# Performance work log

Measured on AMD Instinct MI355X. Metric: run time of the kernel, lower is better.

## Reference

```python
import jax, jax.numpy as jnp
import numpy as np

N = 50000; E = 800000; G = 64
HID = 128; HEADS = 4; HC = HID // HEADS
L = 3; RESID_FREQ = 2
EPS = 1e-5; SLOPE = 0.2


def setup_inputs() -> dict:
    key = jax.random.key(0)
    ks = jax.random.split(key, 16)
    s = 1.0 / np.sqrt(HID)
    f = jnp.float32
    return {
        "x": jax.random.normal(ks[0], (N, HID), f),
        "edge_index": jax.random.randint(ks[1], (2, E), 0, N, dtype=jnp.int32),
        "batch": jnp.sort(jax.random.randint(ks[2], (N,), 0, G, dtype=jnp.int32)),
        "w_in1": jax.random.normal(ks[3], (HID, HID), f) * s,
        "b_in1": jnp.zeros((HID,), f),
        "w_in2": jax.random.normal(ks[4], (HID, HID), f) * s,
        "b_in2": jnp.zeros((HID,), f),
        "gat_w": jax.random.normal(ks[5], (L, HID, HID), f) * s,
        "gat_att_src": jax.random.normal(ks[6], (L, HEADS, HC), f) * s,
        "gat_att_dst": jax.random.normal(ks[7], (L, HEADS, HC), f) * s,
        "gat_b": jnp.zeros((L, HID), f),
        "gcn_w": jax.random.normal(ks[8], (L, HID, HID), f) * s,
        "gcn_b": jnp.zeros((L, HID), f),
        "norm_w": jnp.ones((L, HID), f),
        "norm_b": jnp.zeros((L, HID), f),
        "norm_ms": jnp.ones((L, HID), f),
        "skip_w": jax.random.normal(ks[9], (L, HID, HID), f) * s,
        "skip_b": jnp.zeros((L, HID), f),
        "w_h1": jax.random.normal(ks[10], (HID, HID), f) * s,
        "b_h1": jnp.zeros((HID,), f),
        "w_h2": jax.random.normal(ks[11], (HID, HID // 2), f) * s,
        "b_h2": jnp.zeros((HID // 2,), f),
        "w_h3": jax.random.normal(ks[12], (HID // 2, 1), f) * s,
        "b_h3": jnp.zeros((1,), f),
        "edge_w_param": jnp.ones((1,), f),
    }


def _gat(x, src, dst, w, a_src, a_dst, b):
    # PyG GATConv (eval): lin -> per-edge additive attention -> edge softmax over dst -> scatter-sum
    h = (x @ w).reshape(N, HEADS, HC)
    sc_src = jnp.sum(h * a_src, axis=-1)  # [N, H]
    sc_dst = jnp.sum(h * a_dst, axis=-1)
    alpha = jax.nn.leaky_relu(sc_src[src] + sc_dst[dst], SLOPE)  # [Ef, H]
    amax = jax.ops.segment_max(alpha, dst, num_segments=N)  # every node has a self-loop
    ex = jnp.exp(alpha - amax[dst])
    denom = jax.ops.segment_sum(ex, dst, num_segments=N)
    coef = ex / (denom[dst] + 1e-16)
    out = jax.ops.segment_sum(h[src] * coef[:, :, None], dst, num_segments=N)
    return out.reshape(N, HID) + b


def _gcn(x, src, dst, ew, w, b):
    # PyG GCNConv with improved=True (self-loop weight 2.0 already in ew): sym-normalized SpMM
    deg = jax.ops.segment_sum(ew, dst, num_segments=N)
    dinv = jnp.where(deg > 0, jax.lax.rsqrt(deg), 0.0)
    norm = dinv[src] * ew * dinv[dst]
    h = x @ w
    return jax.ops.segment_sum(h[src] * norm[:, None], dst, num_segments=N) + b


def _graph_norm(x, batch, w, b, ms):
    cnt = jax.ops.segment_sum(jnp.ones((N, 1), x.dtype), batch, num_segments=G)
    cnt = jnp.maximum(cnt, 1.0)
    mean = jax.ops.segment_sum(x, batch, num_segments=G) / cnt
    out = x - mean[batch] * ms
    var = jax.ops.segment_sum(out * out, batch, num_segments=G) / cnt
    return out / jnp.sqrt(var[batch] + EPS) * w + b


def reference(x, edge_index, batch, w_in1, b_in1, w_in2, b_in2, gat_w, gat_att_src,
              gat_att_dst, gat_b, gcn_w, gcn_b, norm_w, norm_b, norm_ms, skip_w,
              skip_b, w_h1, b_h1, w_h2, b_h2, w_h3, b_h3, edge_w_param):
    # undirected: concat reversed edges; then self-loops (added by both GAT and GCN convs)
    loop = jnp.arange(N, dtype=edge_index.dtype)
    src = jnp.concatenate([edge_index[0], edge_index[1], loop])
    dst = jnp.concatenate([edge_index[1], edge_index[0], loop])
    ew = jnp.concatenate([
        edge_w_param[0] * jnp.ones((2 * E,), x.dtype),
        2.0 * jnp.ones((N,), x.dtype),  # improved=True self-loop fill value
    ])
    h = jax.nn.relu(x @ w_in1 + b_in1) @ w_in2 + b_in2
    for i in range(L):
        prev = h
        g1 = _gat(h, src, dst, gat_w[i], gat_att_src[i], gat_att_dst[i], gat_b[i])
        g2 = _gcn(h, src, dst, ew, gcn_w[i], gcn_b[i])
        h = jax.nn.elu(_graph_norm(g1 + g2, batch, norm_w[i], norm_b[i], norm_ms[i]))
        if i % RESID_FREQ == 0:
            h = h + prev @ skip_w[i] + skip_b[i]
    p = jax.nn.relu(h @ w_h1 + b_h1)
    p = jax.nn.relu(p @ w_h2 + b_h2)
    return jax.nn.sigmoid(p @ w_h3 + b_h3).reshape(-1)
```

## Files before the change

kernel.cpp:

```cpp
#include <hip/hip_runtime.h>
#include <hip/hip_fp16.h>

typedef unsigned int uint;
typedef unsigned short ushort;
typedef __attribute__((ext_vector_type(8))) short short8;
typedef __attribute__((ext_vector_type(4))) float f32x4;
typedef __attribute__((ext_vector_type(2))) float f32x2;

#define N_NODES 50000
#define N_EDGES 800000
#define ETOT    (2 * N_EDGES + N_NODES)
#define NG      64
#define NBKT    256
#define MAXB    10240
#define EPB     8192
#define NBK1    ((ETOT + EPB - 1) / EPB)
#define AROW    640

__device__ __forceinline__ short f2bf(float f) {
  uint u = __float_as_uint(f);
  u += 0x7fffu + ((u >> 16) & 1u);
  return (short)(u >> 16);
}
__device__ __forceinline__ float bf2f(short s) {
  return __uint_as_float(((uint)(ushort)s) << 16);
}
__device__ __forceinline__ uint packbf(float a, float b) {
  return (uint)(ushort)f2bf(a) | ((uint)(ushort)f2bf(b) << 16);
}
__device__ __forceinline__ uint pkh2(float a, float b) {
  __half2 h = __floats2half2_rn(a, b);
  return *(uint*)&h;
}
__device__ __forceinline__ float2 uph2(uint u) {
  __half2 h = *(__half2*)&u;
  return __half22float2(h);
}

__global__ __launch_bounds__(256) void bucket_k(const int* __restrict__ ei,
                                                int* __restrict__ gfill,
                                                uint* __restrict__ est) {
  __shared__ int hist[NBKT];
  __shared__ int cursor[NBKT];
  const int tid = threadIdx.x;
  hist[tid] = 0;
  __syncthreads();
  const int e0 = blockIdx.x * EPB;
#pragma unroll 4
  for (int i = 0; i < EPB / 256; ++i) {
    int e = e0 + i * 256 + tid;
    if (e < ETOT) {
      int d;
      if (e < N_EDGES)          d = ei[N_EDGES + e];
      else if (e < 2 * N_EDGES) d = ei[e - N_EDGES];
      else                      d = e - 2 * N_EDGES;
      atomicAdd(&hist[d >> 8], 1);
    }
  }
  __syncthreads();
  cursor[tid] = atomicAdd(&gfill[tid], hist[tid]);
  __syncthreads();
#pragma unroll 4
  for (int i = 0; i < EPB / 256; ++i) {
    int e = e0 + i * 256 + tid;
    if (e < ETOT) {
      int s, d, fl = 0;
      if (e < N_EDGES)          { s = ei[e];           d = ei[N_EDGES + e]; }
      else if (e < 2 * N_EDGES) { s = ei[e];           d = ei[e - N_EDGES]; }
      else                      { s = e - 2 * N_EDGES; d = s; fl = 1; }
      int b = d >> 8;
      int slot = atomicAdd(&cursor[b], 1);
      est[(size_t)b * MAXB + slot] = (uint)s | ((uint)(d & 255) << 16) | ((uint)fl << 24);
    }
  }
}

__global__ __launch_bounds__(256) void group_k(const int* __restrict__ gfill,
                                               const uint* __restrict__ est,
                                               const float* __restrict__ ewp,
                                               int* __restrict__ csrc,
                                               int* __restrict__ rbeg,
                                               int* __restrict__ rend,
                                               float* __restrict__ dinv) {
  __shared__ int hist[NBKT];
  __shared__ int cursor[NBKT];
  __shared__ int wsum[4];
  __shared__ int bsum[4];
  const int b = blockIdx.x;
  const int tid = threadIdx.x;
  const int lane = tid & 63, wid = tid >> 6;
  const int cnt = gfill[b];
  {
    int vv = (tid < b) ? gfill[tid] : 0;
#pragma unroll
    for (int off = 32; off; off >>= 1) vv += __shfl_xor(vv, off, 64);
    if (lane == 0) bsum[wid] = vv;
  }
  hist[tid] = 0;
  __syncthreads();
  const int gb = bsum[0] + bsum[1] + bsum[2] + bsum[3];
  const uint* basep = est + (size_t)b * MAXB;
  for (int i = tid; i < cnt; i += 256)
    atomicAdd(&hist[(basep[i] >> 16) & 255], 1);
  __syncthreads();
  int v = hist[tid];
  int x = v;
#pragma unroll
  for (int d = 1; d < 64; d <<= 1) {
    int t = __shfl_up(x, d, 64);
    if (lane >= d) x += t;
  }
  if (lane == 63) wsum[wid] = x;
  __syncthreads();
  int woff = 0;
#pragma unroll
  for (int j = 0; j < 4; ++j) if (j < wid) woff += wsum[j];
  int excl = woff + x - v;
  cursor[tid] = excl;
  int node = b * 256 + tid;
  if (node < N_NODES) {
    rbeg[node] = gb + excl;
    rend[node] = gb + excl + v;
    float deg = ewp[0] * (float)(v - 1) + 2.0f;
    dinv[node] = (deg > 0.f) ? rsqrtf(deg) : 0.f;
  }
  __syncthreads();
  for (int i = tid; i < cnt; i += 256) {
    uint en = basep[i];
    int dlow = (en >> 16) & 255;
    int slot = atomicAdd(&cursor[dlow], 1);
    csrc[gb + slot] = (int)(en & 0xffffu) | (int)((en >> 24) << 31);
  }
}

__global__ __launch_bounds__(128) void gcnt_k(const int* __restrict__ batch,
                                              int* __restrict__ gcnt) {
  __shared__ int lb[NG + 1];
  int g = threadIdx.x;
  if (g <= NG) {
    int lo = 0, hi = N_NODES;
    while (lo < hi) {
      int mid = (lo + hi) >> 1;
      if (batch[mid] < g) lo = mid + 1; else hi = mid;
    }
    lb[g] = lo;
  }
  __syncthreads();
  if (g < NG) gcnt[g] = lb[g + 1] - lb[g];
}

__global__ __launch_bounds__(256) void prep_k(const float* __restrict__ w_in1,
                                              const float* __restrict__ w_in2,
                                              const float* __restrict__ gat_w,
                                              const float* __restrict__ gcn_w,
                                              const float* __restrict__ skip_w,
                                              const float* __restrict__ w_h1,
                                              const float* __restrict__ w_h2,
                                              short* __restrict__ WT0,
                                              short* __restrict__ WT1,
                                              short* __restrict__ WTL2,
                                              short* __restrict__ WTS,
                                              short* __restrict__ WTH1,
                                              short* __restrict__ WTH2) {
  int mat = blockIdx.x >> 2, qr = blockIdx.x & 3;
  const float* src; short* dst; int ncol = 128, dstride = 128, doff = 0;
  switch (mat) {
    case 0:  src = w_in1; dst = WT0; break;
    case 1:  src = w_in2; dst = WT1; break;
    case 2: case 3: case 4:
      src = gat_w + (size_t)(mat - 2) * 16384; dst = WTL2 + (size_t)(mat - 2) * 32768;
      dstride = 256; break;
    case 5: case 6: case 7:
      src = gcn_w + (size_t)(mat - 5) * 16384; dst = WTL2 + (size_t)(mat - 5) * 32768;
      dstride = 256; doff = 128; break;
    case 8:  src = skip_w;             dst = WTS;         break;
    case 9:  src = skip_w + 2 * 16384; dst = WTS + 16384; break;
    case 10: src = w_h1; dst = WTH1; break;
    default: src = w_h2; dst = WTH2; ncol = 64; break;
  }
  int total = 128 * ncol, chunk = total / 4;
  for (int d = qr * chunk + threadIdx.x; d < (qr + 1) * chunk; d += 256) {
    int col = d >> 7, k = d & 127;
    dst[col * dstride + doff + k] = f2bf(src[k * ncol + col]);
  }
}

__global__ __launch_bounds__(256) void attprep_k(const float* __restrict__ gat_w,
                                                 const float* __restrict__ asrc,
                                                 const float* __restrict__ adst,
                                                 const float* __restrict__ gat_b,
                                                 const float* __restrict__ gcn_b,
                                                 short* __restrict__ ATTW,
                                                 float* __restrict__ BSUM) {
  const int tid = threadIdx.x;
  for (int t = tid; t < 3072; t += 256) {
    int l = t >> 10, rem = t & 1023;
    int r = rem >> 7, k = rem & 127;
    int hd = r & 3;
    const float* av = (r < 4) ? (asrc + l * 128 + hd * 32) : (adst + l * 128 + hd * 32);
    const float* wrow = gat_w + (size_t)l * 16384 + k * 128 + hd * 32;
    float s = 0.f;
#pragma unroll
    for (int c = 0; c < 32; ++c) s = fmaf(wrow[c], av[c], s);
    ATTW[(size_t)l * 2048 + r * 128 + k] = f2bf(s);
  }
  for (int t = tid; t < 3072; t += 256)
    ATTW[(size_t)(t >> 10) * 2048 + 1024 + (t & 1023)] = 0;
  for (int t = tid; t < 384; t += 256) {
    int l = t >> 7, c = t & 127;
    BSUM[t] = gat_b[l * 128 + c] + gcn_b[l * 128 + c];
  }
}

template <int NCOL, int RELU, int F32OUT, int AF32, int NORM>
__global__ __launch_bounds__(256) void bgemm_k(const short* __restrict__ A,
                                               const float* __restrict__ Af,
                                               const short* __restrict__ WT,
                                               const float* __restrict__ bias,
                                               const short* __restrict__ gb_,
                                               const int* __restrict__ batch,
                                               const int* __restrict__ gcnt,
                                               const float* __restrict__ gsum,
                                               const float* __restrict__ nw,
                                               const float* __restrict__ nb_,
                                               const float* __restrict__ nms,
                                               short* __restrict__ outb,
                                               float* __restrict__ outf, int M) {
  constexpr int NT = NCOL / 16;
  const int lane = threadIdx.x & 63;
  const int wid = threadIdx.x >> 6;
  const int mbase = blockIdx.x * 64 + wid * 16;
  const int l15 = lane & 15, q = lane >> 4;
  int arow = mbase + l15; if (arow > M - 1) arow = M - 1;
  const short* bp = WT + (size_t)l15 * 128 + q * 8;
  f32x4 acc[NT];
#pragma unroll
  for (int t = 0; t < NT; ++t) acc[t] = (f32x4)0.f;
#pragma unroll
  for (int c = 0; c < 4; ++c) {
    short8 av;
    if (AF32) {
      const float* apf = Af + (size_t)arow * 128 + q * 8 + c * 32;
      float4 fa = *(const float4*)apf;
      float4 fb = *(const float4*)(apf + 4);
      uint2 lo = make_uint2(packbf(fa.x, fa.y), packbf(fa.z, fa.w));
      uint2 hi = make_uint2(packbf(fb.x, fb.y), packbf(fb.z, fb.w));
      uint4 all = make_uint4(lo.x, lo.y, hi.x, hi.y);
      av = *(short8*)&all;
    } else {
      av = *(const short8*)(A + (size_t)arow * 128 + q * 8 + c * 32);
    }
#pragma unroll
    for (int t = 0; t < NT; ++t) {
      short8 bv = *(const short8*)(bp + (size_t)t * 16 * 128 + c * 32);
      acc[t] = __builtin_amdgcn_mfma_f32_16x16x32_bf16(av, bv, acc[t], 0, 0, 0);
    }
  }
#pragma unroll
  for (int t = 0; t < NT; ++t) {
    int col = t * 16 + l15;
    float bb = bias ? bias[col] : 0.f;
#pragma unroll
    for (int r = 0; r < 4; ++r) {
      int row = mbase + q * 4 + r;
      if (row < M) {
        float v = acc[t][r] + bb;
        if (NORM) {
          int b = batch[row];
          float cinv = 1.0f / fmaxf((float)gcnt[b], 1.0f);
          float mean = gsum[b * 256 + col] * cinv;
          float msq  = gsum[b * 256 + 128 + col] * cinv;
          float ms = nms[col];
          float var = fmaxf(msq - (2.0f * ms - ms * ms) * mean * mean, 0.f);
          float g = bf2f(gb_[(size_t)row * AROW + col]);
          float tn = (g - mean * ms) * rsqrtf(var + 1e-5f) * nw[col] + nb_[col];
          tn = (tn > 0.f) ? tn : (__expf(tn) - 1.0f);
          v += tn;
        }
        if (RELU) v = v > 0.f ? v : 0.f;
        if (F32OUT) outf[(size_t)row * NCOL + col] = v;
        else        outb[(size_t)row * NCOL + col] = f2bf(v);
      }
    }
  }
}

__global__ __launch_bounds__(256) void agg_k(const short* __restrict__ h,
                                             const float* __restrict__ sc,
                                             const int* __restrict__ rbeg,
                                             const int* __restrict__ rend,
                                             const int* __restrict__ cs,
                                             const float* __restrict__ dinv,
                                             const float* __restrict__ ewp,
                                             short* __restrict__ A) {
  __shared__ uint4 lco[4][64];
  const int n = blockIdx.x * 4 + (threadIdx.x >> 6);
  const int wv = threadIdx.x >> 6;
  const int l = threadIdx.x & 63;
  const int sub = l >> 5;
  const int f4 = l & 31;
  const float ew0 = ewp[0];
  const float dn = dinv[n];
  const f32x4 sdv = *(const f32x4*)(sc + n * 16 + 4);
  const int beg = rbeg[n], end = rend[n];
  float den[4] = {0.f, 0.f, 0.f, 0.f};
  f32x2 ag[4][2], ac[2];
#pragma unroll
  for (int hd = 0; hd < 4; ++hd) { ag[hd][0] = (f32x2)0.f; ag[hd][1] = (f32x2)0.f; }
  ac[0] = (f32x2)0.f; ac[1] = (f32x2)0.f;

  for (int c0 = beg; c0 < end; c0 += 64) {
    const int nc = min(64, end - c0);
    {
      uint4 w = make_uint4(0u, 0u, 0u, 0u);
      int e = c0 + l;
      if (e < end) {
        int raw = cs[e];
        int s = raw & 0x7fffffff;
        float wt = (raw < 0) ? 2.0f : ew0;
        f32x4 ssv = *(const f32x4*)(sc + (size_t)s * 16);
        float a0 = ssv[0] + sdv[0]; a0 = fmaxf(a0, 0.2f * a0);
        float a1 = ssv[1] + sdv[1]; a1 = fmaxf(a1, 0.2f * a1);
        float a2 = ssv[2] + sdv[2]; a2 = fmaxf(a2, 0.2f * a2);
        float a3 = ssv[3] + sdv[3]; a3 = fmaxf(a3, 0.2f * a3);
        float e0 = __expf(a0), e1 = __expf(a1);
        float e2 = __expf(a2), e3 = __expf(a3);
        den[0] += e0; den[1] += e1; den[2] += e2; den[3] += e3;
        float c2 = dinv[s] * wt * dn;
        __half hc = __float2half(c2);
        w = make_uint4(pkh2(e0, e1), pkh2(e2, e3),
                       (uint)(*(ushort*)&hc) | ((uint)s << 16), 0u);
      }
      lco[wv][l] = w;
    }
    const int pairs = (nc + 1) & ~1;
#pragma unroll 2
    for (int j = sub; j < pairs; j += 2) {
      uint4 cw = lco[wv][j];
      int s = (int)(cw.z >> 16);
      float2 p01 = uph2(cw.x);
      float2 p23 = uph2(cw.y);
      ushort hc = (ushort)(cw.z & 0xffffu);
      float c2 = __half2float(*(__half*)&hc);
      uint2 u = *(const uint2*)(h + (size_t)s * 128 + f4 * 4);
      f32x2 va, vb;
      va.x = __uint_as_float(u.x << 16);
      va.y = __uint_as_float(u.x & 0xffff0000u);
      vb.x = __uint_as_float(u.y << 16);
      vb.y = __uint_as_float(u.y & 0xffff0000u);
      f32x2 cc;
      cc.x = p01.x; cc.y = p01.x;
      ag[0][0] += cc * va; ag[0][1] += cc * vb;
      cc.x = p01.y; cc.y = p01.y;
      ag[1][0] += cc * va; ag[1][1] += cc * vb;
      cc.x = p23.x; cc.y = p23.x;
      ag[2][0] += cc * va; ag[2][1] += cc * vb;
      cc.x = p23.y; cc.y = p23.y;
      ag[3][0] += cc * va; ag[3][1] += cc * vb;
      cc.x = c2; cc.y = c2;
      ac[0] += cc * va; ac[1] += cc * vb;
    }
  }

#pragma unroll
  for (int off = 1; off < 64; off <<= 1) {
    den[0] += __shfl_xor(den[0], off, 64);
    den[1] += __shfl_xor(den[1], off, 64);
    den[2] += __shfl_xor(den[2], off, 64);
    den[3] += __shfl_xor(den[3], off, 64);
  }
#pragma unroll
  for (int hd = 0; hd < 4; ++hd)
#pragma unroll
    for (int i = 0; i < 2; ++i) {
      f32x2 t = ag[hd][i];
      t.x += __shfl_xor(t.x, 32, 64);
      t.y += __shfl_xor(t.y, 32, 64);
      ag[hd][i] = t;
    }
#pragma unroll
  for (int i = 0; i < 2; ++i) {
    f32x2 t = ac[i];
    t.x += __shfl_xor(t.x, 32, 64);
    t.y += __shfl_xor(t.y, 32, 64);
    ac[i] = t;
  }

  float inv[4] = {1.0f / (den[0] + 1e-16f), 1.0f / (den[1] + 1e-16f),
                  1.0f / (den[2] + 1e-16f), 1.0f / (den[3] + 1e-16f)};
  short* base = A + (size_t)n * AROW;
  if (sub == 0) {
#pragma unroll
    for (int hd = 0; hd < 2; ++hd) {
      float iv = inv[hd];
      *(uint2*)(base + hd * 128 + f4 * 4) =
          make_uint2(packbf(ag[hd][0].x * iv, ag[hd][0].y * iv),
                     packbf(ag[hd][1].x * iv, ag[hd][1].y * iv));
    }
    *(uint2*)(base + 512 + f4 * 4) =
        make_uint2(packbf(ac[0].x, ac[0].y), packbf(ac[1].x, ac[1].y));
  } else {
#pragma unroll
    for (int hd = 2; hd < 4; ++hd) {
      float iv = inv[hd];
      *(uint2*)(base + hd * 128 + f4 * 4) =
          make_uint2(packbf(ag[hd][0].x * iv, ag[hd][0].y * iv),
                     packbf(ag[hd][1].x * iv, ag[hd][1].y * iv));
    }
  }
}

__global__ __launch_bounds__(256) void aggproj_k(const short* A,
                                                 const short* __restrict__ WT,
                                                 const float* __restrict__ bsum,
                                                 short* GB, int M) {
  const int lane = threadIdx.x & 63;
  const int wid = threadIdx.x >> 6;
  const int mbase = blockIdx.x * 64 + wid * 16;
  const int l15 = lane & 15, q = lane >> 4;
  int arow = mbase + l15; if (arow > M - 1) arow = M - 1;
  const short* ap = A + (size_t)arow * AROW + q * 8;
  const short* bp = WT + (size_t)l15 * 256 + q * 8;
  f32x4 acc[8];
#pragma unroll
  for (int t = 0; t < 8; ++t) acc[t] = (f32x4)0.f;
  short8 avg[4];
#pragma unroll
  for (int c = 0; c < 4; ++c) avg[c] = *(const short8*)(ap + 512 + c * 32);
#pragma unroll
  for (int hd = 0; hd < 4; ++hd) {
    short8 avh[4];
#pragma unroll
    for (int c = 0; c < 4; ++c) avh[c] = *(const short8*)(ap + hd * 128 + c * 32);
#pragma unroll
    for (int tt = 0; tt < 2; ++tt) {
      int t = hd * 2 + tt;
      const short* bpt = bp + (size_t)t * 16 * 256;
#pragma unroll
      for (int c = 0; c < 4; ++c) {
        short8 bv = *(const short8*)(bpt + c * 32);
        acc[t] = __builtin_amdgcn_mfma_f32_16x16x32_bf16(avh[c], bv, acc[t], 0, 0, 0);
      }
#pragma unroll
      for (int c = 0; c < 4; ++c) {
        short8 bv = *(const short8*)(bpt + 128 + c * 32);
        acc[t] = __builtin_amdgcn_mfma_f32_16x16x32_bf16(avg[c], bv, acc[t], 0, 0, 0);
      }
    }
  }
#pragma unroll
  for (int t = 0; t < 8; ++t) {
    int col = t * 16 + l15;
    float bb = bsum[col];
#pragma unroll
    for (int r = 0; r < 4; ++r) {
      int row = mbase + q * 4 + r;
      if (row < M) GB[(size_t)row * AROW + col] = f2bf(acc[t][r] + bb);
    }
  }
}

__global__ __launch_bounds__(256) void stats_k(const short* __restrict__ gb,
                                               const int* __restrict__ batch,
                                               float* __restrict__ gsum) {
  int c2 = threadIdx.x & 63;
  int qr = threadIdx.x >> 6;
  int nb = blockIdx.x * 16;
  float s0 = 0.f, s1 = 0.f, q0 = 0.f, q1 = 0.f;
  int curb = -1;
  for (int i = qr; i < 16; i += 4) {
    int n = nb + i;
    int b = batch[n];
    if (b != curb) {
      if (curb >= 0) {
        atomicAdd(&gsum[curb * 256 + 2 * c2], s0);
        atomicAdd(&gsum[curb * 256 + 2 * c2 + 1], s1);
        atomicAdd(&gsum[curb * 256 + 128 + 2 * c2], q0);
        atomicAdd(&gsum[curb * 256 + 128 + 2 * c2 + 1], q1);
      }
      curb = b; s0 = s1 = q0 = q1 = 0.f;
    }
    uint u = *(const uint*)(gb + (size_t)n * AROW + 2 * c2);
    float v0 = __uint_as_float(u << 16);
    float v1 = __uint_as_float(u & 0xffff0000u);
    s0 += v0; q0 = fmaf(v0, v0, q0);
    s1 += v1; q1 = fmaf(v1, v1, q1);
  }
  if (curb >= 0) {
    atomicAdd(&gsum[curb * 256 + 2 * c2], s0);
    atomicAdd(&gsum[curb * 256 + 2 * c2 + 1], s1);
    atomicAdd(&gsum[curb * 256 + 128 + 2 * c2], q0);
    atomicAdd(&gsum[curb * 256 + 128 + 2 * c2 + 1], q1);
  }
}

__global__ __launch_bounds__(256) void normelu_k(const short* __restrict__ gb,
                                                 const int* __restrict__ batch,
                                                 const float* __restrict__ gsum,
                                                 const int* __restrict__ gcnt,
                                                 const float* __restrict__ nw,
                                                 const float* __restrict__ nb_,
                                                 const float* __restrict__ nms,
                                                 short* __restrict__ outb) {
  int n = blockIdx.x * 4 + (threadIdx.x >> 6);
  int c2 = threadIdx.x & 63;
  int b = batch[n];
  float cntf = fmaxf((float)gcnt[b], 1.0f);
  float cinv = 1.0f / cntf;
  uint u = *(const uint*)(gb + (size_t)n * AROW + 2 * c2);
  float o[2];
#pragma unroll
  for (int k = 0; k < 2; ++k) {
    int c = 2 * c2 + k;
    float mean = gsum[b * 256 + c] * cinv;
    float msq  = gsum[b * 256 + 128 + c] * cinv;
    float ms = nms[c];
    float var = fmaxf(msq - (2.0f * ms - ms * ms) * mean * mean, 0.f);
    float v = (k == 0) ? __uint_as_float(u << 16) : __uint_as_float(u & 0xffff0000u);
    float t = (v - mean * ms) * rsqrtf(var + 1e-5f) * nw[c] + nb_[c];
    o[k] = (t > 0.f) ? t : (__expf(t) - 1.0f);
  }
  *(uint*)(outb + (size_t)n * 128 + 2 * c2) = packbf(o[0], o[1]);
}

__global__ __launch_bounds__(256) void head3_k(const short* __restrict__ p2,
                                               const float* __restrict__ w3,
                                               const float* __restrict__ b3,
                                               float* __restrict__ out) {
  int n = blockIdx.x * 4 + (threadIdx.x >> 6);
  int k = threadIdx.x & 63;
  float v = bf2f(p2[(size_t)n * 64 + k]) * w3[k];
#pragma unroll
  for (int off = 32; off; off >>= 1) v += __shfl_down(v, off, 64);
  if (k == 0) out[n] = 1.0f / (1.0f + __expf(-(v + b3[0])));
}

extern "C" void kernel_launch(void* const* d_in, const int* in_sizes, int n_in,
                              void* d_out, int out_size, void* d_ws, size_t ws_size,
                              hipStream_t stream) {
  const float* x      = (const float*)d_in[0];
  const int*   ei     = (const int*)d_in[1];
  const int*   batch  = (const int*)d_in[2];
  const float* w_in1  = (const float*)d_in[3];
  const float* b_in1  = (const float*)d_in[4];
  const float* w_in2  = (const float*)d_in[5];
  const float* b_in2  = (const float*)d_in[6];
  const float* gat_w  = (const float*)d_in[7];
  const float* gat_as = (const float*)d_in[8];
  const float* gat_ad = (const float*)d_in[9];
  const float* gat_b  = (const float*)d_in[10];
  const float* gcn_w  = (const float*)d_in[11];
  const float* gcn_b  = (const float*)d_in[12];
  const float* norm_w = (const float*)d_in[13];
  const float* norm_b = (const float*)d_in[14];
  const float* norm_ms= (const float*)d_in[15];
  const float* skip_w = (const float*)d_in[16];
  const float* skip_b = (const float*)d_in[17];
  const float* w_h1   = (const float*)d_in[18];
  const float* b_h1   = (const float*)d_in[19];
  const float* w_h2   = (const float*)d_in[20];
  const float* b_h2   = (const float*)d_in[21];
  const float* w_h3   = (const float*)d_in[22];
  const float* b_h3   = (const float*)d_in[23];
  const float* ewp    = (const float*)d_in[24];
  float* out = (float*)d_out;

  char* p = (char*)d_ws;
  const size_t NBH = (size_t)N_NODES * 128 * sizeof(short);
  short* B0   = (short*)p; p += NBH;
  short* B1   = (short*)p; p += NBH;
  short* MEGA = (short*)p; p += (size_t)N_NODES * AROW * sizeof(short);
  short* GB   = MEGA;
  uint*  EST  = (uint*)MEGA;
  float* SC   = (float*)p; p += (size_t)N_NODES * 16 * sizeof(float);
  int*   CSRC = (int*)p;   p += (size_t)ETOT * sizeof(int);
  int*   RBEG = (int*)p;   p += (size_t)N_NODES * sizeof(int);
  int*   REND = (int*)p;   p += (size_t)N_NODES * sizeof(int);
  char*  zbase = p;
  int*   GFILL= (int*)p;   p += (size_t)NBKT * sizeof(int);
  float* GSUM = (float*)p; p += (size_t)3 * NG * 256 * sizeof(float);
  size_t znb  = (size_t)((char*)p - zbase);
  int*   GCNT = (int*)p;   p += (size_t)NG * sizeof(int);
  float* DINV = (float*)p; p += (size_t)N_NODES * sizeof(float);
  short* WT0  = (short*)p; p += 16384 * sizeof(short);
  short* WT1  = (short*)p; p += 16384 * sizeof(short);
  short* WTL2 = (short*)p; p += 3 * 32768 * sizeof(short);
  short* WTS  = (short*)p; p += 2 * 16384 * sizeof(short);
  short* WTH1 = (short*)p; p += 16384 * sizeof(short);
  short* WTH2 = (short*)p; p += 8192 * sizeof(short);
  short* ATTW = (short*)p; p += 3 * 2048 * sizeof(short);
  float* BSUM = (float*)p; p += 3 * 128 * sizeof(float);

  const int GB_ = (N_NODES + 63) / 64;
  const short* nullb = nullptr;

  hipMemsetAsync(zbase, 0, znb, stream);
  bucket_k<<<NBK1, 256, 0, stream>>>(ei, GFILL, EST);
  group_k<<<196, 256, 0, stream>>>(GFILL, EST, ewp, CSRC, RBEG, REND, DINV);
  gcnt_k<<<1, 128, 0, stream>>>(batch, GCNT);
  prep_k<<<48, 256, 0, stream>>>(w_in1, w_in2, gat_w, gcn_w, skip_w, w_h1, w_h2,
                                 WT0, WT1, WTL2, WTS, WTH1, WTH2);
  attprep_k<<<1, 256, 0, stream>>>(gat_w, gat_as, gat_ad, gat_b, gcn_b, ATTW, BSUM);

  bgemm_k<128, 1, 0, 1, 0><<<GB_, 256, 0, stream>>>(nullb, x, WT0, b_in1,
      nullb, nullptr, nullptr, nullptr, nullptr, nullptr, nullptr, B1, nullptr, N_NODES);
  bgemm_k<128, 0, 0, 0, 0><<<GB_, 256, 0, stream>>>(B1, nullptr, WT1, b_in2,
      nullb, nullptr, nullptr, nullptr, nullptr, nullptr, nullptr, B0, nullptr, N_NODES);

  short* h = B0;
  for (int i = 0; i < 3; ++i) {
    short* hn = (h == B0) ? B1 : B0;
    float* gsum_i = GSUM + (size_t)i * NG * 256;
    const float* nw  = norm_w  + (size_t)i * 128;
    const float* nb  = norm_b  + (size_t)i * 128;
    const float* nms = norm_ms + (size_t)i * 128;
    bgemm_k<16, 0, 1, 0, 0><<<GB_, 256, 0, stream>>>(h, nullptr,
        ATTW + (size_t)i * 2048, nullptr, nullb, nullptr, nullptr, nullptr,
        nullptr, nullptr, nullptr, nullptr, SC, N_NODES);
    agg_k<<<N_NODES / 4, 256, 0, stream>>>(h, SC, RBEG, REND, CSRC, DINV, ewp, MEGA);
    aggproj_k<<<GB_, 256, 0, stream>>>(MEGA, WTL2 + (size_t)i * 32768,
                                       BSUM + i * 128, GB, N_NODES);
    stats_k<<<N_NODES / 16, 256, 0, stream>>>(GB, batch, gsum_i);
    if (i == 1) {
      normelu_k<<<N_NODES / 4, 256, 0, stream>>>(GB, batch, gsum_i, GCNT,
                                                 nw, nb, nms, hn);
    } else {
      const short* wts = WTS + (size_t)(i == 0 ? 0 : 1) * 16384;
      bgemm_k<128, 0, 0, 0, 1><<<GB_, 256, 0, stream>>>(h, nullptr, wts,
          skip_b + (size_t)i * 128, GB, batch, GCNT, gsum_i, nw, nb, nms,
          hn, nullptr, N_NODES);
    }
    h = hn;
  }

  bgemm_k<128, 1, 0, 0, 0><<<GB_, 256, 0, stream>>>(h, nullptr, WTH1, b_h1,
      nullb, nullptr, nullptr, nullptr, nullptr, nullptr, nullptr, B0, nullptr, N_NODES);
  bgemm_k<64, 1, 0, 0, 0><<<GB_, 256, 0, stream>>>(B0, nullptr, WTH2, b_h2,
      nullb, nullptr, nullptr, nullptr, nullptr, nullptr, nullptr, MEGA, nullptr, N_NODES);
  head3_k<<<N_NODES / 4, 256, 0, stream>>>(MEGA, w_h3, b_h3, out);
}
```

Baseline: 856.0 us.

## Fuse input MLP and head GEMMs, merge prep kernels, stage edge bucketing in LDS

The two input-MLP GEMMs become one kernel that keeps the hidden layer in shared memory, and the head's three stages (two GEMMs plus the final dot product and sigmoid) become one kernel. The three small prep kernels are merged into a single launch. Edge bucketing now handles only the real edges: self-loops are written directly by group_k, and entries are staged in LDS in bucket order so the global writes are contiguous. The goal is fewer launches, no intermediate activation round-trips through global memory, and more coalesced scatter writes, at the cost of extra shared-memory use and more complex index bookkeeping.

Result: faster. 813.3 us (-5.0%).

```diff
diff --git a/kernel.cpp b/kernel.cpp
--- a/kernel.cpp
+++ b/kernel.cpp
@@ -9,12 +9,13 @@
 
 #define N_NODES 50000
 #define N_EDGES 800000
+#define EREAL   (2 * N_EDGES)
 #define ETOT    (2 * N_EDGES + N_NODES)
 #define NG      64
 #define NBKT    256
 #define MAXB    10240
 #define EPB     8192
-#define NBK1    ((ETOT + EPB - 1) / EPB)
+#define NBK1    ((EREAL + EPB - 1) / EPB)
 #define AROW    640
 
 __device__ __forceinline__ short f2bf(float f) {
@@ -41,37 +42,54 @@
                                                 int* __restrict__ gfill,
                                                 uint* __restrict__ est) {
   __shared__ int hist[NBKT];
-  __shared__ int cursor[NBKT];
+  __shared__ int scan_[NBKT];
+  __shared__ int cur[NBKT];
+  __shared__ int claim[NBKT];
+  __shared__ int wsum[4];
+  __shared__ uint stage[EPB];
   const int tid = threadIdx.x;
   hist[tid] = 0;
   __syncthreads();
   const int e0 = blockIdx.x * EPB;
-#pragma unroll 4
-  for (int i = 0; i < EPB / 256; ++i) {
-    int e = e0 + i * 256 + tid;
-    if (e < ETOT) {
-      int d;
-      if (e < N_EDGES)          d = ei[N_EDGES + e];
-      else if (e < 2 * N_EDGES) d = ei[e - N_EDGES];
-      else                      d = e - 2 * N_EDGES;
-      atomicAdd(&hist[d >> 8], 1);
-    }
-  }
-  __syncthreads();
-  cursor[tid] = atomicAdd(&gfill[tid], hist[tid]);
-  __syncthreads();
-#pragma unroll 4
-  for (int i = 0; i < EPB / 256; ++i) {
-    int e = e0 + i * 256 + tid;
-    if (e < ETOT) {
-      int s, d, fl = 0;
-      if (e < N_EDGES)          { s = ei[e];           d = ei[N_EDGES + e]; }
-      else if (e < 2 * N_EDGES) { s = ei[e];           d = ei[e - N_EDGES]; }
-      else                      { s = e - 2 * N_EDGES; d = s; fl = 1; }
-      int b = d >> 8;
-      int slot = atomicAdd(&cursor[b], 1);
-      est[(size_t)b * MAXB + slot] = (uint)s | ((uint)(d & 255) << 16) | ((uint)fl << 24);
-    }
+  const int ecnt = min(EPB, EREAL - e0);
+  for (int i = tid; i < ecnt; i += 256) {
+    int e = e0 + i;
+    int d = (e < N_EDGES) ? ei[N_EDGES + e] : ei[e - N_EDGES];
+    atomicAdd(&hist[d >> 8], 1);
+  }
+  __syncthreads();
+  {
+    int v = hist[tid];
+    int lane = tid & 63, wid = tid >> 6;
+    int x = v;
+#pragma unroll
+    for (int d = 1; d < 64; d <<= 1) {
+      int t = __shfl_up(x, d, 64);
+      if (lane >= d) x += t;
+    }
+    if (lane == 63) wsum[wid] = x;
+    __syncthreads();
+    int woff = 0;
+#pragma unroll
+    for (int j = 0; j < 4; ++j) if (j < wid) woff += wsum[j];
+    scan_[tid] = woff + x - v;
+    cur[tid] = woff + x - v;
+    claim[tid] = atomicAdd(&gfill[tid], v);
+  }
+  __syncthreads();
+  for (int i = tid; i < ecnt; i += 256) {
+    int e = e0 + i;
+    int s = ei[e];
+    int d = (e < N_EDGES) ? ei[N_EDGES + e] : ei[e - N_EDGES];
+    int p = atomicAdd(&cur[d >> 8], 1);
+    stage[p] = (uint)s | ((uint)d << 16);
+  }
+  __syncthreads();
+  for (int p = tid; p < ecnt; p += 256) {
+    uint en = stage[p];
+    int b = en >> 24;
+    int gpos = claim[b] + (p - scan_[b]);
+    est[(size_t)b * MAXB + gpos] = en;
   }
 }
 
@@ -98,7 +116,7 @@
   }
   hist[tid] = 0;
   __syncthreads();
-  const int gb = bsum[0] + bsum[1] + bsum[2] + bsum[3];
+  const int gb = bsum[0] + bsum[1] + bsum[2] + bsum[3] + b * 256;
   const uint* basep = est + (size_t)b * MAXB;
   for (int i = tid; i < cnt; i += 256)
     atomicAdd(&hist[(basep[i] >> 16) & 255], 1);
@@ -116,12 +134,14 @@
 #pragma unroll
   for (int j = 0; j < 4; ++j) if (j < wid) woff += wsum[j];
   int excl = woff + x - v;
-  cursor[tid] = excl;
+  cursor[tid] = excl + tid + 1;
   int node = b * 256 + tid;
   if (node < N_NODES) {
-    rbeg[node] = gb + excl;
-    rend[node] = gb + excl + v;
-    float deg = ewp[0] * (float)(v - 1) + 2.0f;
+    int rs = gb + excl + tid;
+    rbeg[node] = rs;
+    rend[node] = rs + v + 1;
+    csrc[rs] = node | (int)0x80000000;
+    float deg = ewp[0] * (float)v + 2.0f;
     dinv[node] = (deg > 0.f) ? rsqrtf(deg) : 0.f;
   }
   __syncthreads();
@@ -129,39 +149,67 @@
     uint en = basep[i];
     int dlow = (en >> 16) & 255;
     int slot = atomicAdd(&cursor[dlow], 1);
-    csrc[gb + slot] = (int)(en & 0xffffu) | (int)((en >> 24) << 31);
-  }
-}
-
-__global__ __launch_bounds__(128) void gcnt_k(const int* __restrict__ batch,
-                                              int* __restrict__ gcnt) {
+    csrc[gb + slot] = (int)(en & 0xffffu);
+  }
+}
+
+__global__ __launch_bounds__(256) void prepall_k(const float* __restrict__ w_in1,
+                                                 const float* __restrict__ w_in2,
+                                                 const float* __restrict__ gat_w,
+                                                 const float* __restrict__ gcn_w,
+                                                 const float* __restrict__ skip_w,
+                                                 const float* __restrict__ w_h1,
+                                                 const float* __restrict__ w_h2,
+                                                 const float* __restrict__ asrc,
+                                                 const float* __restrict__ adst,
+                                                 const float* __restrict__ gat_b,
+                                                 const float* __restrict__ gcn_b,
+                                                 const int* __restrict__ batch,
+                                                 short* __restrict__ WT0,
+                                                 short* __restrict__ WT1,
+                                                 short* __restrict__ WTL2,
+                                                 short* __restrict__ WTS,
+                                                 short* __restrict__ WTH1,
+                                                 short* __restrict__ WTH2,
+                                                 short* __restrict__ ATTW,
+                                                 float* __restrict__ BSUM,
+                                                 int* __restrict__ gcnt) {
   __shared__ int lb[NG + 1];
-  int g = threadIdx.x;
-  if (g <= NG) {
-    int lo = 0, hi = N_NODES;
-    while (lo < hi) {
-      int mid = (lo + hi) >> 1;
-      if (batch[mid] < g) lo = mid + 1; else hi = mid;
-    }
-    lb[g] = lo;
-  }
-  __syncthreads();
-  if (g < NG) gcnt[g] = lb[g + 1] - lb[g];
-}
-
-__global__ __launch_bounds__(256) void prep_k(const float* __restrict__ w_in1,
-                                              const float* __restrict__ w_in2,
-                                              const float* __restrict__ gat_w,
-                                              const float* __restrict__ gcn_w,
-                                              const float* __restrict__ skip_w,
-                                              const float* __restrict__ w_h1,
-                                              const float* __restrict__ w_h2,
-                                              short* __restrict__ WT0,
-                                              short* __restrict__ WT1,
-                                              short* __restrict__ WTL2,
-                                              short* __restrict__ WTS,
-                                              short* __restrict__ WTH1,
-                                              short* __restrict__ WTH2) {
+  const int tid = threadIdx.x;
+  if (blockIdx.x == 48) {
+    for (int t = tid; t < 3072; t += 256) {
+      int l = t >> 10, rem = t & 1023;
+      int r = rem >> 7, k = rem & 127;
+      int hd = r & 3;
+      const float* av = (r < 4) ? (asrc + l * 128 + hd * 32) : (adst + l * 128 + hd * 32);
+      const float* wrow = gat_w + (size_t)l * 16384 + k * 128 + hd * 32;
+      float s = 0.f;
+#pragma unroll
+      for (int c = 0; c < 32; ++c) s = fmaf(wrow[c], av[c], s);
+      ATTW[(size_t)l * 2048 + r * 128 + k] = f2bf(s);
+    }
+    for (int t = tid; t < 3072; t += 256)
+      ATTW[(size_t)(t >> 10) * 2048 + 1024 + (t & 1023)] = 0;
+    for (int t = tid; t < 384; t += 256) {
+      int l = t >> 7, c = t & 127;
+      BSUM[t] = gat_b[l * 128 + c] + gcn_b[l * 128 + c];
+    }
+    return;
+  }
+  if (blockIdx.x == 49) {
+    int g = tid;
+    if (g <= NG) {
+      int lo = 0, hi = N_NODES;
+      while (lo < hi) {
+        int mid = (lo + hi) >> 1;
+        if (batch[mid] < g) lo = mid + 1; else hi = mid;
+      }
+      lb[g] = lo;
+    }
+    __syncthreads();
+    if (g < NG) gcnt[g] = lb[g + 1] - lb[g];
+    return;
+  }
   int mat = blockIdx.x >> 2, qr = blockIdx.x & 3;
   const float* src; short* dst; int ncol = 128, dstride = 128, doff = 0;
   switch (mat) {
@@ -179,42 +227,14 @@
     default: src = w_h2; dst = WTH2; ncol = 64; break;
   }
   int total = 128 * ncol, chunk = total / 4;
-  for (int d = qr * chunk + threadIdx.x; d < (qr + 1) * chunk; d += 256) {
+  for (int d = qr * chunk + tid; d < (qr + 1) * chunk; d += 256) {
     int col = d >> 7, k = d & 127;
     dst[col * dstride + doff + k] = f2bf(src[k * ncol + col]);
   }
 }
 
-__global__ __launch_bounds__(256) void attprep_k(const float* __restrict__ gat_w,
-                                                 const float* __restrict__ asrc,
-                                                 const float* __restrict__ adst,
-                                                 const float* __restrict__ gat_b,
-                                                 const float* __restrict__ gcn_b,
-                                                 short* __restrict__ ATTW,
-                                                 float* __restrict__ BSUM) {
-  const int tid = threadIdx.x;
-  for (int t = tid; t < 3072; t += 256) {
-    int l = t >> 10, rem = t & 1023;
-    int r = rem >> 7, k = rem & 127;
-    int hd = r & 3;
-    const float* av = (r < 4) ? (asrc + l * 128 + hd * 32) : (adst + l * 128 + hd * 32);
-    const float* wrow = gat_w + (size_t)l * 16384 + k * 128 + hd * 32;
-    float s = 0.f;
-#pragma unroll
-    for (int c = 0; c < 32; ++c) s = fmaf(wrow[c], av[c], s);
-    ATTW[(size_t)l * 2048 + r * 128 + k] = f2bf(s);
-  }
-  for (int t = tid; t < 3072; t += 256)
-    ATTW[(size_t)(t >> 10) * 2048 + 1024 + (t & 1023)] = 0;
-  for (int t = tid; t < 384; t += 256) {
-    int l = t >> 7, c = t & 127;
-    BSUM[t] = gat_b[l * 128 + c] + gcn_b[l * 128 + c];
-  }
-}
-
-template <int NCOL, int RELU, int F32OUT, int AF32, int NORM>
+template <int NCOL, int RELU, int F32OUT, int NORM>
 __global__ __launch_bounds__(256) void bgemm_k(const short* __restrict__ A,
-                                               const float* __restrict__ Af,
                                                const short* __restrict__ WT,
                                                const float* __restrict__ bias,
                                                const short* __restrict__ gb_,
@@ -232,24 +252,14 @@
   const int mbase = blockIdx.x * 64 + wid * 16;
   const int l15 = lane & 15, q = lane >> 4;
   int arow = mbase + l15; if (arow > M - 1) arow = M - 1;
+  const short* ap = A + (size_t)arow * 128 + q * 8;
   const short* bp = WT + (size_t)l15 * 128 + q * 8;
   f32x4 acc[NT];
 #pragma unroll
   for (int t = 0; t < NT; ++t) acc[t] = (f32x4)0.f;
 #pragma unroll
   for (int c = 0; c < 4; ++c) {
-    short8 av;
-    if (AF32) {
-      const float* apf = Af + (size_t)arow * 128 + q * 8 + c * 32;
-      float4 fa = *(const float4*)apf;
-      float4 fb = *(const float4*)(apf + 4);
-      uint2 lo = make_uint2(packbf(fa.x, fa.y), packbf(fa.z, fa.w));
-      uint2 hi = make_uint2(packbf(fb.x, fb.y), packbf(fb.z, fb.w));
-      uint4 all = make_uint4(lo.x, lo.y, hi.x, hi.y);
-      av = *(short8*)&all;
-    } else {
-      av = *(const short8*)(A + (size_t)arow * 128 + q * 8 + c * 32);
-    }
+    short8 av = *(const short8*)(ap + c * 32);
 #pragma unroll
     for (int t = 0; t < NT; ++t) {
       short8 bv = *(const short8*)(bp + (size_t)t * 16 * 128 + c * 32);
@@ -281,6 +291,154 @@
         if (F32OUT) outf[(size_t)row * NCOL + col] = v;
         else        outb[(size_t)row * NCOL + col] = f2bf(v);
       }
+    }
+  }
+}
+
+__global__ __launch_bounds__(256) void mlp2_k(const float* __restrict__ x,
+                                              const short* __restrict__ WT0,
+                                              const float* __restrict__ b1,
+                                              const short* __restrict__ WT1,
+                                              const float* __restrict__ b2,
+                                              short* __restrict__ outb, int M) {
+  __shared__ short sh[64][136];
+  const int lane = threadIdx.x & 63;
+  const int wid = threadIdx.x >> 6;
+  const int mbase = blockIdx.x * 64 + wid * 16;
+  const int l15 = lane & 15, q = lane >> 4;
+  int arow = mbase + l15; if (arow > M - 1) arow = M - 1;
+  f32x4 acc[8];
+#pragma unroll
+  for (int t = 0; t < 8; ++t) acc[t] = (f32x4)0.f;
+#pragma unroll
+  for (int c = 0; c < 4; ++c) {
+    const float* apf = x + (size_t)arow * 128 + q * 8 + c * 32;
+    float4 fa = *(const float4*)apf;
+    float4 fb = *(const float4*)(apf + 4);
+    uint4 all = make_uint4(packbf(fa.x, fa.y), packbf(fa.z, fa.w),
+                           packbf(fb.x, fb.y), packbf(fb.z, fb.w));
+    short8 av = *(short8*)&all;
+    const short* bp = WT0 + (size_t)l15 * 128 + q * 8 + c * 32;
+#pragma unroll
+    for (int t = 0; t < 8; ++t) {
+      short8 bv = *(const short8*)(bp + (size_t)t * 16 * 128);
+      acc[t] = __builtin_amdgcn_mfma_f32_16x16x32_bf16(av, bv, acc[t], 0, 0, 0);
+    }
+  }
+#pragma unroll
+  for (int t = 0; t < 8; ++t) {
+    int col = t * 16 + l15;
+    float bb = b1[col];
+#pragma unroll
+    for (int r = 0; r < 4; ++r) {
+      float v = acc[t][r] + bb;
+      sh[wid * 16 + q * 4 + r][col] = f2bf(v > 0.f ? v : 0.f);
+    }
+  }
+  __syncthreads();
+  f32x4 acc2[8];
+#pragma unroll
+  for (int t = 0; t < 8; ++t) acc2[t] = (f32x4)0.f;
+  const short* ap2 = &sh[wid * 16 + l15][0] + q * 8;
+#pragma unroll
+  for (int c = 0; c < 4; ++c) {
+    short8 av = *(const short8*)(ap2 + c * 32);
+    const short* bp = WT1 + (size_t)l15 * 128 + q * 8 + c * 32;
+#pragma unroll
+    for (int t = 0; t < 8; ++t) {
+      short8 bv = *(const short8*)(bp + (size_t)t * 16 * 128);
+      acc2[t] = __builtin_amdgcn_mfma_f32_16x16x32_bf16(av, bv, acc2[t], 0, 0, 0);
+    }
+  }
+#pragma unroll
+  for (int t = 0; t < 8; ++t) {
+    int col = t * 16 + l15;
+    float bb = b2[col];
+#pragma unroll
+    for (int r = 0; r < 4; ++r) {
+      int row = mbase + q * 4 + r;
+      if (row < M) outb[(size_t)row * 128 + col] = f2bf(acc2[t][r] + bb);
+    }
+  }
+}
+
+__global__ __launch_bounds__(256) void head_k(const short* __restrict__ h,
+                                              const short* __restrict__ WTH1,
+                                              const float* __restrict__ b1,
+                                              const short* __restrict__ WTH2,
+                                              const float* __restrict__ b2,
+                                              const float* __restrict__ w3,
+                                              const float* __restrict__ b3,
+                                              float* __restrict__ out, int M) {
+  __shared__ short sh[64][136];
+  const int lane = threadIdx.x & 63;
+  const int wid = threadIdx.x >> 6;
+  const int mbase = blockIdx.x * 64 + wid * 16;
+  const int l15 = lane & 15, q = lane >> 4;
+  int arow = mbase + l15; if (arow > M - 1) arow = M - 1;
+  const short* ap = h + (size_t)arow * 128 + q * 8;
+  f32x4 acc[8];
+#pragma unroll
+  for (int t = 0; t < 8; ++t) acc[t] = (f32x4)0.f;
+#pragma unroll
+  for (int c = 0; c < 4; ++c) {
+    short8 av = *(const short8*)(ap + c * 32);
+    const short* bp = WTH1 + (size_t)l15 * 128 + q * 8 + c * 32;
+#pragma unroll
+    for (int t = 0; t < 8; ++t) {
+      short8 bv = *(const short8*)(bp + (size_t)t * 16 * 128);
+      acc[t] = __builtin_amdgcn_mfma_f32_16x16x32_bf16(av, bv, acc[t], 0, 0, 0);
+    }
+  }
+#pragma unroll
+  for (int t = 0; t < 8; ++t) {
+    int col = t * 16 + l15;
+    float bb = b1[col];
+#pragma unroll
+    for (int r = 0; r < 4; ++r) {
+      float v = acc[t][r] + bb;
+      sh[wid * 16 + q * 4 + r][col] = f2bf(v > 0.f ? v : 0.f);
+    }
+  }
+  __syncthreads();
+  f32x4 p2[4];
+#pragma unroll
+  for (int t = 0; t < 4; ++t) p2[t] = (f32x4)0.f;
+  const short* ap2 = &sh[wid * 16 + l15][0] + q * 8;
+#pragma unroll
+  for (int c = 0; c < 4; ++c) {
+    short8 av = *(const short8*)(ap2 + c * 32);
+    const short* bp = WTH2 + (size_t)l15 * 128 + q * 8 + c * 32;
+#pragma unroll
+    for (int t = 0; t < 4; ++t) {
+      short8 bv = *(const short8*)(bp + (size_t)t * 16 * 128);
+      p2[t] = __builtin_amdgcn_mfma_f32_16x16x32_bf16(av, bv, p2[t], 0, 0, 0);
+    }
+  }
+  float w3v[4];
+#pragma unroll
+  for (int t = 0; t < 4; ++t) w3v[t] = w3[t * 16 + l15];
+  float rsum[4];
+#pragma unroll
+  for (int r = 0; r < 4; ++r) {
+    float s = 0.f;
+#pragma unroll
+    for (int t = 0; t < 4; ++t) {
+      float v = p2[t][r] + b2[t * 16 + l15];
+      v = v > 0.f ? v : 0.f;
+      s = fmaf(v, w3v[t], s);
+    }
+    rsum[r] = s;
+  }
+#pragma unroll
+  for (int off = 1; off < 16; off <<= 1)
+#pragma unroll
+    for (int r = 0; r < 4; ++r) rsum[r] += __shfl_xor(rsum[r], off, 64);
+  if (l15 == 0) {
+#pragma unroll
+    for (int r = 0; r < 4; ++r) {
+      int row = mbase + q * 4 + r;
+      if (row < M) out[row] = 1.0f / (1.0f + __expf(-(rsum[r] + b3[0])));
     }
   }
 }
@@ -521,18 +679,6 @@
     o[k] = (t > 0.f) ? t : (__expf(t) - 1.0f);
   }
   *(uint*)(outb + (size_t)n * 128 + 2 * c2) = packbf(o[0], o[1]);
-}
-
-__global__ __launch_bounds__(256) void head3_k(const short* __restrict__ p2,
-                                               const float* __restrict__ w3,
-                                               const float* __restrict__ b3,
-                                               float* __restrict__ out) {
-  int n = blockIdx.x * 4 + (threadIdx.x >> 6);
-  int k = threadIdx.x & 63;
-  float v = bf2f(p2[(size_t)n * 64 + k]) * w3[k];
-#pragma unroll
-  for (int off = 32; off; off >>= 1) v += __shfl_down(v, off, 64);
-  if (k == 0) out[n] = 1.0f / (1.0f + __expf(-(v + b3[0])));
 }
 
 extern "C" void kernel_launch(void* const* d_in, const int* in_sizes, int n_in,
@@ -597,15 +743,12 @@
   hipMemsetAsync(zbase, 0, znb, stream);
   bucket_k<<<NBK1, 256, 0, stream>>>(ei, GFILL, EST);
   group_k<<<196, 256, 0, stream>>>(GFILL, EST, ewp, CSRC, RBEG, REND, DINV);
-  gcnt_k<<<1, 128, 0, stream>>>(batch, GCNT);
-  prep_k<<<48, 256, 0, stream>>>(w_in1, w_in2, gat_w, gcn_w, skip_w, w_h1, w_h2,
-                                 WT0, WT1, WTL2, WTS, WTH1, WTH2);
-  attprep_k<<<1, 256, 0, stream>>>(gat_w, gat_as, gat_ad, gat_b, gcn_b, ATTW, BSUM);
-
-  bgemm_k<128, 1, 0, 1, 0><<<GB_, 256, 0, stream>>>(nullb, x, WT0, b_in1,
-      nullb, nullptr, nullptr, nullptr, nullptr, nullptr, nullptr, B1, nullptr, N_NODES);
-  bgemm_k<128, 0, 0, 0, 0><<<GB_, 256, 0, stream>>>(B1, nullptr, WT1, b_in2,
-      nullb, nullptr, nullptr, nullptr, nullptr, nullptr, nullptr, B0, nullptr, N_NODES);
+  prepall_k<<<50, 256, 0, stream>>>(w_in1, w_in2, gat_w, gcn_w, skip_w, w_h1,
+                                    w_h2, gat_as, gat_ad, gat_b, gcn_b, batch,
+                                    WT0, WT1, WTL2, WTS, WTH1, WTH2, ATTW,
+                                    BSUM, GCNT);
+
+  mlp2_k<<<GB_, 256, 0, stream>>>(x, WT0, b_in1, WT1, b_in2, B0, N_NODES);
 
   short* h = B0;
   for (int i = 0; i < 3; ++i) {
@@ -614,9 +757,9 @@
     const float* nw  = norm_w  + (size_t)i * 128;
     const float* nb  = norm_b  + (size_t)i * 128;
     const float* nms = norm_ms + (size_t)i * 128;
-    bgemm_k<16, 0, 1, 0, 0><<<GB_, 256, 0, stream>>>(h, nullptr,
-        ATTW + (size_t)i * 2048, nullptr, nullb, nullptr, nullptr, nullptr,
-        nullptr, nullptr, nullptr, nullptr, SC, N_NODES);
+    bgemm_k<16, 0, 1, 0><<<GB_, 256, 0, stream>>>(h, ATTW + (size_t)i * 2048,
+        nullptr, nullb, nullptr, nullptr, nullptr, nullptr, nullptr, nullptr,
+        nullptr, SC, N_NODES);
     agg_k<<<N_NODES / 4, 256, 0, stream>>>(h, SC, RBEG, REND, CSRC, DINV, ewp, MEGA);
     aggproj_k<<<GB_, 256, 0, stream>>>(MEGA, WTL2 + (size_t)i * 32768,
                                        BSUM + i * 128, GB, N_NODES);
@@ -626,16 +769,13 @@
                                                  nw, nb, nms, hn);
     } else {
       const short* wts = WTS + (size_t)(i == 0 ? 0 : 1) * 16384;
-      bgemm_k<128, 0, 0, 0, 1><<<GB_, 256, 0, stream>>>(h, nullptr, wts,
+      bgemm_k<128, 0, 0, 1><<<GB_, 256, 0, stream>>>(h, wts,
           skip_b + (size_t)i * 128, GB, batch, GCNT, gsum_i, nw, nb, nms,
           hn, nullptr, N_NODES);
     }
     h = hn;
   }
 
-  bgemm_k<128, 1, 0, 0, 0><<<GB_, 256, 0, stream>>>(h, nullptr, WTH1, b_h1,
-      nullb, nullptr, nullptr, nullptr, nullptr, nullptr, nullptr, B0, nullptr, N_NODES);
-  bgemm_k<64, 1, 0, 0, 0><<<GB_, 256, 0, stream>>>(B0, nullptr, WTH2, b_h2,
-      nullb, nullptr, nullptr, nullptr, nullptr, nullptr, nullptr, MEGA, nullptr, N_NODES);
-  head3_k<<<N_NODES / 4, 256, 0, stream>>>(MEGA, w_h3, b_h3, out);
-}
+  head_k<<<GB_, 256, 0, stream>>>(h, WTH1, b_h1, WTH2, b_h2, w_h3, b_h3, out,
+                                  N_NODES);
+}
```
